# Kernel tuning notes

Hardware: AMD Instinct MI355X
Metric: run time of the kernel (lower is better)

## Reference

```python
import jax, jax.numpy as jnp
import numpy as np


def _lstm(x, h0, c0, Wih, Whh, b):
    """Single-layer LSTM, batch_first input x: [B,T,D]. PyTorch gate order i,f,g,o.
    Returns (h_seq [T,B,H], h_T [B,H], c_T [B,H])."""
    xs = jnp.swapaxes(x, 0, 1)  # [T,B,D]

    def step(carry, xt):
        h, c = carry
        gates = xt @ Wih.T + h @ Whh.T + b  # [B,4H]
        i, f, g, o = jnp.split(gates, 4, axis=-1)
        c = jax.nn.sigmoid(f) * c + jax.nn.sigmoid(i) * jnp.tanh(g)
        h = jax.nn.sigmoid(o) * jnp.tanh(c)
        return (h, c), h

    (h, c), hs = jax.lax.scan(step, (h0, c0), xs)
    return hs, h, c


def setup_inputs() -> dict:
    key = jax.random.key(0)
    ks = jax.random.split(key, 16)
    B, T, Tf, Tu = 256, 365, 15, 76
    Dh, Df, Du, H = 64, 32, 16, 256
    s = 1.0 / np.sqrt(H)  # torch-style uniform scale, approximated with scaled normals
    return {
        "x_d": jax.random.normal(ks[0], (B, T, Dh), jnp.float32),
        "x_f": jax.random.normal(ks[1], (B, Tf, Df), jnp.float32),
        "x_ff": jax.random.normal(ks[2], (B, Tu, Du), jnp.float32),
        "enc_Wih": jax.random.normal(ks[3], (4 * H, Dh), jnp.float32) * s,
        "enc_Whh": jax.random.normal(ks[4], (4 * H, H), jnp.float32) * s,
        "enc_b": jax.random.normal(ks[5], (4 * H,), jnp.float32) * s,
        "decf_Wih": jax.random.normal(ks[6], (4 * H, Df), jnp.float32) * s,
        "decf_Whh": jax.random.normal(ks[7], (4 * H, H), jnp.float32) * s,
        "decf_b": jax.random.normal(ks[8], (4 * H,), jnp.float32) * s,
        "decu_Wih": jax.random.normal(ks[9], (4 * H, Du), jnp.float32) * s,
        "decu_Whh": jax.random.normal(ks[10], (4 * H, H), jnp.float32) * s,
        "decu_b": jax.random.normal(ks[11], (4 * H,), jnp.float32) * s,
        "head_W": jax.random.normal(ks[12], (1, H), jnp.float32) * s,
        "head_b": jax.random.normal(ks[13], (1,), jnp.float32) * s,
    }


def reference(x_d, x_f, x_ff, enc_Wih, enc_Whh, enc_b,
              decf_Wih, decf_Whh, decf_b, decu_Wih, decu_Whh, decu_b,
              head_W, head_b):
    B = x_d.shape[0]
    H = enc_Whh.shape[1]
    Tf = x_f.shape[1]
    Tu = x_ff.shape[1]
    horizon = Tf + Tu
    h0 = jnp.zeros((B, H), x_d.dtype)
    c0 = jnp.zeros((B, H), x_d.dtype)

    # Encoder over historical sequence
    _, h, c = _lstm(x_d, h0, c0, enc_Wih, enc_Whh, enc_b)

    # Forecast decoder: one LSTM step per horizon step + linear head (dropout = eval identity)
    hs_f, h, c = _lstm(x_f, h, c, decf_Wih, decf_Whh, decf_b)  # [Tf,B,H]
    out_f = (jnp.einsum('tbh,oh->tbo', hs_f, head_W)[..., 0] + head_b[0]).T  # [B,Tf]

    # Future decoder, continuing the hidden state
    hs_u, h, c = _lstm(x_ff, h, c, decu_Wih, decu_Whh, decu_b)  # [Tu,B,H]
    out_u = (jnp.einsum('tbh,oh->tbo', hs_u, head_W)[..., 0] + head_b[0]).T  # [B,Tu]

    # Faithful to original: both loops write outputs[:, t], so the future loop
    # overwrites the first Tu columns.
    outputs = jnp.zeros((B, horizon), x_d.dtype)
    outputs = outputs.at[:, :Tf].set(out_f)
    outputs = outputs.at[:, :Tu].set(out_u)
    return outputs
```

## Files before the change

kernel.cpp:

```cpp
#include <hip/hip_runtime.h>
#include <stdint.h>


typedef __attribute__((ext_vector_type(8))) short short8;
typedef __attribute__((ext_vector_type(4))) float f32x4;
typedef __attribute__((ext_vector_type(2))) unsigned int u32x2;

#define L2E 1.4426950408889634f

__device__ __forceinline__ uint16_t f2bf(float f) {
  uint32_t x = __float_as_uint(f);
  x += 0x7fffu + ((x >> 16) & 1u);
  return (uint16_t)(x >> 16);
}
__device__ __forceinline__ uint32_t pk2(float a, float b) {
  return (uint32_t)f2bf(a) | ((uint32_t)f2bf(b) << 16);
}
__device__ __forceinline__ uint32_t cvtpk(float lo, float hi) {
  uint32_t r;
  asm("v_cvt_pk_bf16_f32 %0, %1, %2" : "=v"(r) : "v"(lo), "v"(hi));
  return r;
}
__device__ __forceinline__ float bfhalf(uint32_t w, int hi) {
  return __uint_as_float(hi ? (w & 0xffff0000u) : (w << 16));
}
__device__ __forceinline__ f32x4 MFMA(short8 a, short8 b, f32x4 c) {
  return __builtin_amdgcn_mfma_f32_16x16x32_bf16(a, b, c, 0, 0, 0);
}
__device__ __forceinline__ float ex2(float x) { return __builtin_amdgcn_exp2f(x); }
__device__ __forceinline__ float rcp(float x) { return __builtin_amdgcn_rcpf(x); }

__device__ __forceinline__ void lgkm_barrier() {
  __builtin_amdgcn_sched_barrier(0);
  asm volatile("s_waitcnt lgkmcnt(0)" ::: "memory");
  __builtin_amdgcn_s_barrier();
  __builtin_amdgcn_sched_barrier(0);
}
__device__ __forceinline__ void vm_drain4() {
  __builtin_amdgcn_sched_barrier(0);
  asm volatile("s_waitcnt vmcnt(4)" ::: "memory");
  __builtin_amdgcn_sched_barrier(0);
}

__global__ void init_kernel(float* c_state, uint16_t* h_state, float* out,
                            uint32_t* flags) {
  int i = blockIdx.x * 256 + threadIdx.x;
  if (i < 65536) { c_state[i] = 0.f; h_state[i] = 0; }
  if (i < 256 * 91) out[i] = 0.f;
  if (i < 96) flags[i] = 0;
}

template <int DIN>
__global__ __launch_bounds__(512) void xproj_kernel(
    const float* __restrict__ x, const float* __restrict__ Wih,
    const float* __restrict__ bias, uint32_t* __restrict__ xp,
    int t0, int T) {
  const int tid = threadIdx.x, w = tid >> 6, l = tid & 63;
  const int l16 = l & 15, lg = l >> 4;
  const int tc = blockIdx.x >> 1;
  const int sub = blockIdx.x & 1;
  const int t = t0 + tc;
  constexpr int KT = (DIN + 31) / 32;

  short8 bfr[8][KT];
  float4 bias4[8];
#pragma unroll
  for (int ni = 0; ni < 8; ++ni) {
    const int n = (w * 8 + ni) * 16 + l16;
    bias4[ni] = *(const float4*)&bias[(w * 8 + ni) * 16 + lg * 4];
#pragma unroll
    for (int kt = 0; kt < KT; ++kt) {
      const int k0 = kt * 32 + lg * 8;
      short8 fr;
#pragma unroll
      for (int e = 0; e < 8; ++e) fr[e] = 0;
      if (k0 + 8 <= DIN) {
        const float* s = Wih + (size_t)n * DIN + k0;
#pragma unroll
        for (int e = 0; e < 8; ++e) fr[e] = (short)f2bf(s[e]);
      }
      bfr[ni][kt] = fr;
    }
  }

  for (int mi = 0; mi < 8; ++mi) {
    const int btile = sub * 8 + mi;
    const int b = btile * 16 + l16;
    short8 af[KT];
#pragma unroll
    for (int kt = 0; kt < KT; ++kt) {
      const int k0 = kt * 32 + lg * 8;
      short8 fr;
#pragma unroll
      for (int e = 0; e < 8; ++e) fr[e] = 0;
      if (k0 + 8 <= DIN) {
        const float* s = x + ((size_t)b * T + t) * DIN + k0;
#pragma unroll
        for (int e = 0; e < 8; ++e) fr[e] = (short)f2bf(s[e]);
      }
      af[kt] = fr;
    }
#pragma unroll
    for (int ni = 0; ni < 8; ++ni) {
      f32x4 acc = {0.f, 0.f, 0.f, 0.f};
#pragma unroll
      for (int kt = 0; kt < KT; ++kt) acc = MFMA(bfr[ni][kt], af[kt], acc);
      const int nt = w * 8 + ni;
      const float sc = ((nt >> 4) == 2) ? (2.f * L2E) : -L2E;
      size_t idx = ((((size_t)tc * 16 + btile) * 64 + nt) * 64 + l) * 2;
      u32x2 v;
      v[0] = pk2((acc[0] + bias4[ni].x) * sc, (acc[1] + bias4[ni].y) * sc);
      v[1] = pk2((acc[2] + bias4[ni].z) * sc, (acc[3] + bias4[ni].w) * sc);
      *(u32x2*)(xp + idx) = v;
    }
  }
}

template <int DO_HEAD>
__global__ __launch_bounds__(512, 2) void rec_kernel(
    const uint32_t* __restrict__ xp, const float* __restrict__ Whh,
    float* __restrict__ c_state, uint16_t* __restrict__ h_state,
    float* __restrict__ out, const float* __restrict__ headW,
    const float* __restrict__ headb, uint32_t* __restrict__ flags,
    unsigned long long* __restrict__ hx, uint32_t* __restrict__ hxh,
    int ct, int t0, int phase) {
  __shared__ short8 B_lds[64 * 64];
  __shared__ uint16_t h_lds[2][16][264];
  __shared__ float headbuf[16][8];

  const int tid = threadIdx.x, w = tid >> 6, l = tid & 63;
  const int l16 = l & 15, lg = l >> 4;
  const int blk = blockIdx.x;
  const int pair = blk & 15, s = blk >> 4, sp = 1 - s;
  const int b0 = pair * 16;
  const int ctile = s * 8 + w;
  uint32_t* const pflag = flags + (phase * 16 + pair) * 2 + sp;
  uint32_t* const myflag = flags + (phase * 16 + pair) * 2 + s;

  short8 bv[24];
#pragma unroll
  for (int g = 0; g < 4; ++g) {
    const float wsc = (g == 2) ? (2.f * L2E) : -L2E;
#pragma unroll
    for (int kk = 0; kk < 8; ++kk) {
      const int kt = (kk < 4) ? (4 * s + kk) : (4 * sp + (kk - 4));
      const int row = (g * 16 + ctile) * 16 + l16;
      const float* sw = Whh + (size_t)row * 256 + kt * 32 + lg * 8;
      short8 fr;
#pragma unroll
      for (int e = 0; e < 8; ++e) fr[e] = (short)f2bf(sw[e] * wsc);
      if (kk <= 5) bv[g * 6 + kk] = fr;
      else B_lds[(w * 8 + g * 2 + (kk - 6)) * 64 + l] = fr;
    }
  }

  float c_reg[4];
  {
    float4 c4 = *(const float4*)&c_state[(size_t)(b0 + l16) * 256 +
                                         ctile * 16 + lg * 4];
    c_reg[0] = c4.x; c_reg[1] = c4.y; c_reg[2] = c4.z; c_reg[3] = c4.w;
  }
  for (int idx = tid; idx < 16 * 256; idx += 512)
    h_lds[0][idx >> 8][idx & 255] = h_state[(size_t)(b0 + (idx >> 8)) * 256 + (idx & 255)];
  float4 hw4 = *(const float4*)&headW[ctile * 16 + lg * 4];
  const float hb = headb[0];

  const uint32_t* xpb = xp + ((size_t)(pair * 64 + ctile) * 64 + l) * 2;
  u32x2 xpf[4];
#pragma unroll
  for (int g = 0; g < 4; ++g)
    xpf[g] = *(const u32x2*)(xpb + (size_t)g * 2048);

  __syncthreads();

  u32x2 h_last;
  h_last[0] = 0; h_last[1] = 0;
  float hsum_prev = 0.f;

  for (int t = 0; t < ct; ++t) {
    const int cur = t & 1, nxt = cur ^ 1;
    const int tn = (t + 1 < ct) ? t + 1 : t;
    const int par = t & 1;

    unsigned long long pv = 0ull;
    if (t > 0) {
      const uint32_t tgt = (uint32_t)(t0 + t);
      __builtin_amdgcn_sched_barrier(0);
      uint32_t f;
      do {
        f = __hip_atomic_load(pflag, __ATOMIC_RELAXED, __HIP_MEMORY_SCOPE_AGENT);
      } while ((int)(f - tgt) < 0);
      __builtin_amdgcn_sched_barrier(0);
      pv = __hip_atomic_load(
          hx + ((size_t)((pair * 2 + sp) * 2 + ((t - 1) & 1)) * 512) +
              (w * 4 + lg) * 16 + l16,
          __ATOMIC_RELAXED, __HIP_MEMORY_SCOPE_AGENT);
      if (DO_HEAD && s == 0 && tid < 16) {
        uint32_t pp = __hip_atomic_load(
            hxh + ((pair * 2 + sp) * 2 + ((t - 1) & 1)) * 16 + tid,
            __ATOMIC_RELAXED, __HIP_MEMORY_SCOPE_AGENT);
        out[(size_t)(b0 + tid) * 91 + (t0 + t - 1)] =
            hsum_prev + __uint_as_float(pp) + hb;
      }
    }

    f32x4 acc[4];
#pragma unroll
    for (int g = 0; g < 4; ++g) {
      f32x4 ai;
      ai[0] = bfhalf(xpf[g][0], 0);
      ai[1] = bfhalf(xpf[g][0], 1);
      ai[2] = bfhalf(xpf[g][1], 0);
      ai[3] = bfhalf(xpf[g][1], 1);
      acc[g] = ai;
    }
#pragma unroll
    for (int kk = 0; kk < 4; ++kk) {
      short8 hf = *(const short8*)(&h_lds[cur][l16][(4 * s + kk) * 32 + lg * 8]);
#pragma unroll
      for (int g = 0; g < 4; ++g)
        acc[g] = MFMA(bv[g * 6 + kk], hf, acc[g]);
    }

    if (t > 0) {
      u32x2 pw;
      pw[0] = (uint32_t)pv;
      pw[1] = (uint32_t)(pv >> 32);
      *(u32x2*)(&h_lds[cur][l16][sp * 128 + w * 16 + lg * 4]) = pw;
      lgkm_barrier();
    }

#pragma unroll
    for (int kk = 0; kk < 4; ++kk) {
      short8 hf = *(const short8*)(&h_lds[cur][l16][(4 * sp + kk) * 32 + lg * 8]);
#pragma unroll
      for (int g = 0; g < 4; ++g) {
        if (kk < 2) acc[g] = MFMA(bv[g * 6 + 4 + kk], hf, acc[g]);
        else acc[g] = MFMA(B_lds[(w * 8 + g * 2 + (kk - 2)) * 64 + l], hf, acc[g]);
      }
    }

    float hv[4];
#pragma unroll
    for (int j = 0; j < 4; ++j) {
      float ei = ex2(acc[0][j]);
      float ef = ex2(acc[1][j]);
      float eg = ex2(acc[2][j]);
      float eo = ex2(acc[3][j]);
      float eip = 1.f + ei, egp = eg + 1.f, efp = 1.f + ef;
      float d1 = eip * egp;
      float R = rcp(d1 * efp);
      float sitg = (eg - 1.f) * efp * R;
      float cc = fmaf(c_reg[j] * d1, R, sitg);
      c_reg[j] = cc;
      float ec = ex2(cc * (2.f * L2E));
      float hh = (ec - 1.f) * rcp((1.f + eo) * (ec + 1.f));
      hv[j] = hh;
    }

    h_last[0] = cvtpk(hv[0], hv[1]);
    h_last[1] = cvtpk(hv[2], hv[3]);
    *(u32x2*)(&h_lds[nxt][l16][ctile * 16 + lg * 4]) = h_last;
    {
      unsigned long long v64 =
          ((unsigned long long)h_last[1] << 32) | (unsigned long long)h_last[0];
      __hip_atomic_store(
          hx + ((size_t)((pair * 2 + s) * 2 + par) * 512) + (w * 4 + lg) * 16 + l16,
          v64, __ATOMIC_RELAXED, __HIP_MEMORY_SCOPE_AGENT);
    }

#pragma unroll
    for (int g = 0; g < 4; ++g)
      xpf[g] = *(const u32x2*)(xpb + (size_t)tn * 131072 + g * 2048);

    if (DO_HEAD) {
      float hp = fmaf(hv[0], hw4.x, fmaf(hv[1], hw4.y,
                 fmaf(hv[2], hw4.z, hv[3] * hw4.w)));
      hp += __shfl_xor(hp, 16);
      hp += __shfl_xor(hp, 32);
      if (lg == 0) headbuf[l16][w] = hp;
    }

    vm_drain4();
    lgkm_barrier();

    if (DO_HEAD) {
      if (tid < 16) {
        const float* hbp = headbuf[tid];
        hsum_prev = hbp[0] + hbp[1] + hbp[2] + hbp[3] +
                    hbp[4] + hbp[5] + hbp[6] + hbp[7];
        __hip_atomic_store(hxh + ((pair * 2 + s) * 2 + par) * 16 + tid,
                           __float_as_uint(hsum_prev), __ATOMIC_RELAXED,
                           __HIP_MEMORY_SCOPE_AGENT);
      }
      vm_drain4();
    }
    if (tid == 0)
      __hip_atomic_store(myflag, (uint32_t)(t0 + t + 1), __ATOMIC_RELAXED,
                         __HIP_MEMORY_SCOPE_AGENT);
  }

  {
    float4 c4 = {c_reg[0], c_reg[1], c_reg[2], c_reg[3]};
    *(float4*)&c_state[(size_t)(b0 + l16) * 256 + ctile * 16 + lg * 4] = c4;
  }

  if (s == 0) {
    const uint32_t tgt = (uint32_t)(t0 + ct);
    __builtin_amdgcn_sched_barrier(0);
    uint32_t f;
    do {
      f = __hip_atomic_load(pflag, __ATOMIC_RELAXED, __HIP_MEMORY_SCOPE_AGENT);
    } while ((int)(f - tgt) < 0);
    __builtin_amdgcn_sched_barrier(0);
    unsigned long long pv = __hip_atomic_load(
        hx + ((size_t)((pair * 2 + sp) * 2 + ((ct - 1) & 1)) * 512) +
            (w * 4 + lg) * 16 + l16,
        __ATOMIC_RELAXED, __HIP_MEMORY_SCOPE_AGENT);
    u32x2 pw;
    pw[0] = (uint32_t)pv;
    pw[1] = (uint32_t)(pv >> 32);
    *(u32x2*)&h_state[(size_t)(b0 + l16) * 256 + 128 + w * 16 + lg * 4] = pw;
    *(u32x2*)&h_state[(size_t)(b0 + l16) * 256 + w * 16 + lg * 4] = h_last;
    if (DO_HEAD && tid < 16) {
      uint32_t pp = __hip_atomic_load(
          hxh + ((pair * 2 + sp) * 2 + ((ct - 1) & 1)) * 16 + tid,
          __ATOMIC_RELAXED, __HIP_MEMORY_SCOPE_AGENT);
      out[(size_t)(b0 + tid) * 91 + (t0 + ct - 1)] =
          hsum_prev + __uint_as_float(pp) + hb;
    }
  }
}

extern "C" void kernel_launch(void* const* d_in, const int* in_sizes, int n_in,
                              void* d_out, int out_size, void* d_ws, size_t ws_size,
                              hipStream_t stream) {
  const float* headW = (const float*)d_in[12];
  const float* headb = (const float*)d_in[13];
  float* out = (float*)d_out;

  char* ws = (char*)d_ws;
  float* c_state = (float*)ws;
  uint16_t* h_state = (uint16_t*)(ws + 262144);
  uint32_t* flags = (uint32_t*)(ws + 393216);
  unsigned long long* hx = (unsigned long long*)(ws + 397312);
  uint32_t* hxh = (uint32_t*)(ws + 659456);
  uint32_t* xp = (uint32_t*)(ws + 667648);

  int ct_max = 1;
  if (ws_size > 667648 + 512 * 1024) {
    size_t c = (ws_size - 667648) / (512 * 1024);
    ct_max = (c > 365) ? 365 : (int)c;
  }

  init_kernel<<<256, 256, 0, stream>>>(c_state, h_state, out, flags);

  struct Phase { const float* x; const float* Wih; const float* Whh; const float* b; int T; int D; int head; };
  Phase ph[3] = {
      {(const float*)d_in[0], (const float*)d_in[3], (const float*)d_in[4], (const float*)d_in[5],
       in_sizes[0] / (256 * 64), 64, 0},
      {(const float*)d_in[1], (const float*)d_in[6], (const float*)d_in[7], (const float*)d_in[8],
       in_sizes[1] / (256 * 32), 32, 0},
      {(const float*)d_in[2], (const float*)d_in[9], (const float*)d_in[10], (const float*)d_in[11],
       in_sizes[2] / (256 * 16), 16, 1},
  };

  for (int pi = 0; pi < 3; ++pi) {
    const Phase& P = ph[pi];
    for (int t0 = 0; t0 < P.T; t0 += ct_max) {
      int ct = (P.T - t0 < ct_max) ? (P.T - t0) : ct_max;
      dim3 g(ct * 2);
      if (P.D == 64)
        xproj_kernel<64><<<g, 512, 0, stream>>>(P.x, P.Wih, P.b, xp, t0, P.T);
      else if (P.D == 32)
        xproj_kernel<32><<<g, 512, 0, stream>>>(P.x, P.Wih, P.b, xp, t0, P.T);
      else
        xproj_kernel<16><<<g, 512, 0, stream>>>(P.x, P.Wih, P.b, xp, t0, P.T);
      if (P.head)
        rec_kernel<1><<<32, 512, 0, stream>>>(xp, P.Whh, c_state, h_state, out,
                                              headW, headb, flags, hx, hxh,
                                              ct, t0, pi);
      else
        rec_kernel<0><<<32, 512, 0, stream>>>(xp, P.Whh, c_state, h_state, out,
                                              headW, headb, flags, hx, hxh,
                                              ct, t0, pi);
    }
  }
}
```

Baseline: 1.248 ms.

## Run encoder recurrence on single-block-per-batch-tile kernel without cross-block flags

Adds a new recurrence kernel in which one 512-thread block owns a 16-row batch tile and computes all 1024 gate columns itself. Most of W_hh is held in registers, two K-tiles live in LDS, and h is exchanged only through LDS double buffering. This removes the inter-block flag handshake of the split version for the long encoder phase. When workspace allows, all three input projections are precomputed up front, and the decoders keep the split kernel. The input-projection packing also switches to vectorized float4 loads with the hardware bf16 convert. The trade-off is half the blocks (16 instead of 32), so each block carries twice the MFMA work per step and more register pressure.

```diff
diff --git a/kernel.cpp b/kernel.cpp
--- a/kernel.cpp
+++ b/kernel.cpp
@@ -5,6 +5,7 @@
 typedef __attribute__((ext_vector_type(8))) short short8;
 typedef __attribute__((ext_vector_type(4))) float f32x4;
 typedef __attribute__((ext_vector_type(2))) unsigned int u32x2;
+typedef __attribute__((ext_vector_type(4))) unsigned int u32x4;
 
 #define L2E 1.4426950408889634f
 
@@ -13,9 +14,6 @@
   x += 0x7fffu + ((x >> 16) & 1u);
   return (uint16_t)(x >> 16);
 }
-__device__ __forceinline__ uint32_t pk2(float a, float b) {
-  return (uint32_t)f2bf(a) | ((uint32_t)f2bf(b) << 16);
-}
 __device__ __forceinline__ uint32_t cvtpk(float lo, float hi) {
   uint32_t r;
   asm("v_cvt_pk_bf16_f32 %0, %1, %2" : "=v"(r) : "v"(lo), "v"(hi));
@@ -29,6 +27,16 @@
 }
 __device__ __forceinline__ float ex2(float x) { return __builtin_amdgcn_exp2f(x); }
 __device__ __forceinline__ float rcp(float x) { return __builtin_amdgcn_rcpf(x); }
+
+__device__ __forceinline__ short8 pack8s(const float* s, float sc) {
+  float4 q0 = *(const float4*)s, q1 = *(const float4*)(s + 4);
+  u32x4 t;
+  t[0] = cvtpk(q0.x * sc, q0.y * sc);
+  t[1] = cvtpk(q0.z * sc, q0.w * sc);
+  t[2] = cvtpk(q1.x * sc, q1.y * sc);
+  t[3] = cvtpk(q1.z * sc, q1.w * sc);
+  return *(short8*)&t;
+}
 
 __device__ __forceinline__ void lgkm_barrier() {
   __builtin_amdgcn_sched_barrier(0);
@@ -47,7 +55,7 @@
   int i = blockIdx.x * 256 + threadIdx.x;
   if (i < 65536) { c_state[i] = 0.f; h_state[i] = 0; }
   if (i < 256 * 91) out[i] = 0.f;
-  if (i < 96) flags[i] = 0;
+  if (flags && i < 96) flags[i] = 0;
 }
 
 template <int DIN>
@@ -74,11 +82,7 @@
       short8 fr;
 #pragma unroll
       for (int e = 0; e < 8; ++e) fr[e] = 0;
-      if (k0 + 8 <= DIN) {
-        const float* s = Wih + (size_t)n * DIN + k0;
-#pragma unroll
-        for (int e = 0; e < 8; ++e) fr[e] = (short)f2bf(s[e]);
-      }
+      if (k0 + 8 <= DIN) fr = pack8s(Wih + (size_t)n * DIN + k0, 1.f);
       bfr[ni][kt] = fr;
     }
   }
@@ -93,11 +97,7 @@
       short8 fr;
 #pragma unroll
       for (int e = 0; e < 8; ++e) fr[e] = 0;
-      if (k0 + 8 <= DIN) {
-        const float* s = x + ((size_t)b * T + t) * DIN + k0;
-#pragma unroll
-        for (int e = 0; e < 8; ++e) fr[e] = (short)f2bf(s[e]);
-      }
+      if (k0 + 8 <= DIN) fr = pack8s(x + ((size_t)b * T + t) * DIN + k0, 1.f);
       af[kt] = fr;
     }
 #pragma unroll
@@ -109,8 +109,8 @@
       const float sc = ((nt >> 4) == 2) ? (2.f * L2E) : -L2E;
       size_t idx = ((((size_t)tc * 16 + btile) * 64 + nt) * 64 + l) * 2;
       u32x2 v;
-      v[0] = pk2((acc[0] + bias4[ni].x) * sc, (acc[1] + bias4[ni].y) * sc);
-      v[1] = pk2((acc[2] + bias4[ni].z) * sc, (acc[3] + bias4[ni].w) * sc);
+      v[0] = cvtpk((acc[0] + bias4[ni].x) * sc, (acc[1] + bias4[ni].y) * sc);
+      v[1] = cvtpk((acc[2] + bias4[ni].z) * sc, (acc[3] + bias4[ni].w) * sc);
       *(u32x2*)(xp + idx) = v;
     }
   }
@@ -118,6 +118,156 @@
 
 template <int DO_HEAD>
 __global__ __launch_bounds__(512, 2) void rec_kernel(
+    const uint32_t* __restrict__ xp, const float* __restrict__ Whh,
+    float* __restrict__ c_state, uint16_t* __restrict__ h_state,
+    float* __restrict__ out, const float* __restrict__ headW,
+    const float* __restrict__ headb, int ct, int tcol0) {
+  __shared__ short8 B_lds[8 * 16 * 64];
+  __shared__ uint16_t h_lds[2][16][264];
+  __shared__ float headbuf[2][16][8];
+
+  const int tid = threadIdx.x, w = tid >> 6, l = tid & 63;
+  const int l16 = l & 15, lg = l >> 4;
+  const int blk = blockIdx.x, b0 = blk * 16;
+
+  short8 bv[48];
+#pragma unroll
+  for (int g = 0; g < 4; ++g) {
+    const float wsc = (g == 2) ? (2.f * L2E) : -L2E;
+#pragma unroll
+    for (int nt = 0; nt < 2; ++nt)
+#pragma unroll
+      for (int kt = 0; kt < 8; ++kt) {
+        const int row = (g * 16 + w * 2 + nt) * 16 + l16;
+        const float* s = Whh + (size_t)row * 256 + kt * 32 + lg * 8;
+        short8 fr;
+#pragma unroll
+        for (int e = 0; e < 8; ++e) fr[e] = (short)f2bf(s[e] * wsc);
+        const int tile = g * 2 + nt;
+        if (kt <= 5) bv[tile * 6 + kt] = fr;
+        else B_lds[(w * 16 + (kt - 6) * 8 + tile) * 64 + l] = fr;
+      }
+  }
+
+  float c_reg[2][4];
+#pragma unroll
+  for (int nt = 0; nt < 2; ++nt) {
+    float4 c4 = *(const float4*)&c_state[(size_t)(b0 + l16) * 256 +
+                                         (w * 2 + nt) * 16 + lg * 4];
+    c_reg[nt][0] = c4.x; c_reg[nt][1] = c4.y;
+    c_reg[nt][2] = c4.z; c_reg[nt][3] = c4.w;
+  }
+  for (int idx = tid; idx < 16 * 256; idx += 512)
+    h_lds[0][idx >> 8][idx & 255] = h_state[(size_t)(b0 + (idx >> 8)) * 256 + (idx & 255)];
+  float4 hw4[2];
+#pragma unroll
+  for (int nt = 0; nt < 2; ++nt)
+    hw4[nt] = *(const float4*)&headW[(w * 2 + nt) * 16 + lg * 4];
+  const float hb = headb[0];
+
+  const uint32_t* xpb = xp + ((size_t)(blk * 64 + w * 2) * 64 + l) * 2;
+  u32x2 xpf[2][4];
+#pragma unroll
+  for (int nt = 0; nt < 2; ++nt)
+#pragma unroll
+    for (int g = 0; g < 4; ++g)
+      xpf[nt][g] = *(const u32x2*)(xpb + (size_t)g * 2048 + nt * 128);
+
+  __syncthreads();
+
+  for (int t = 0; t < ct; ++t) {
+    const int cur = t & 1, nxt = cur ^ 1;
+    const int tn = (t + 1 < ct) ? t + 1 : t;
+    float hp = 0.f;
+
+#pragma unroll
+    for (int nt = 0; nt < 2; ++nt) {
+      f32x4 acc[4];
+#pragma unroll
+      for (int g = 0; g < 4; ++g) {
+        f32x4 ai;
+        ai[0] = bfhalf(xpf[nt][g][0], 0);
+        ai[1] = bfhalf(xpf[nt][g][0], 1);
+        ai[2] = bfhalf(xpf[nt][g][1], 0);
+        ai[3] = bfhalf(xpf[nt][g][1], 1);
+        acc[g] = ai;
+      }
+#pragma unroll
+      for (int kt = 0; kt <= 5; ++kt) {
+        short8 hf = *(const short8*)(&h_lds[cur][l16][kt * 32 + lg * 8]);
+#pragma unroll
+        for (int g = 0; g < 4; ++g)
+          acc[g] = MFMA(bv[(g * 2 + nt) * 6 + kt], hf, acc[g]);
+      }
+#pragma unroll
+      for (int kt = 6; kt <= 7; ++kt) {
+        short8 hf = *(const short8*)(&h_lds[cur][l16][kt * 32 + lg * 8]);
+#pragma unroll
+        for (int g = 0; g < 4; ++g)
+          acc[g] = MFMA(B_lds[(w * 16 + (kt - 6) * 8 + g * 2 + nt) * 64 + l], hf, acc[g]);
+      }
+
+      float hv[4];
+#pragma unroll
+      for (int j = 0; j < 4; ++j) {
+        float ei = ex2(acc[0][j]);
+        float ef = ex2(acc[1][j]);
+        float eg = ex2(acc[2][j]);
+        float eo = ex2(acc[3][j]);
+        float eip = 1.f + ei, egp = eg + 1.f, efp = 1.f + ef;
+        float d1 = eip * egp;
+        float R = rcp(d1 * efp);
+        float sitg = (eg - 1.f) * efp * R;
+        float cc = fmaf(c_reg[nt][j] * d1, R, sitg);
+        c_reg[nt][j] = cc;
+        float ec = ex2(cc * (2.f * L2E));
+        float hh = (ec - 1.f) * rcp((1.f + eo) * (ec + 1.f));
+        hv[j] = hh;
+      }
+      if (DO_HEAD) {
+        hp = fmaf(hv[0], hw4[nt].x, hp); hp = fmaf(hv[1], hw4[nt].y, hp);
+        hp = fmaf(hv[2], hw4[nt].z, hp); hp = fmaf(hv[3], hw4[nt].w, hp);
+      }
+      {
+        u32x2 hwrd;
+        hwrd[0] = cvtpk(hv[0], hv[1]);
+        hwrd[1] = cvtpk(hv[2], hv[3]);
+        *(u32x2*)(&h_lds[nxt][l16][(w * 2 + nt) * 16 + lg * 4]) = hwrd;
+      }
+#pragma unroll
+      for (int g = 0; g < 4; ++g)
+        xpf[nt][g] = *(const u32x2*)(xpb + (size_t)tn * 131072 + g * 2048 + nt * 128);
+    }
+
+    if (DO_HEAD) {
+      float s = hp;
+      s += __shfl_xor(s, 16);
+      s += __shfl_xor(s, 32);
+      if (lg == 0) headbuf[t & 1][l16][w] = s;
+    }
+
+    lgkm_barrier();
+
+    if (DO_HEAD) {
+      if (tid < 16) {
+        const float* hbp = headbuf[t & 1][tid];
+        float s = hbp[0] + hbp[1] + hbp[2] + hbp[3] + hbp[4] + hbp[5] + hbp[6] + hbp[7];
+        out[(size_t)(b0 + tid) * 91 + (tcol0 + t)] = s + hb;
+      }
+    }
+  }
+
+#pragma unroll
+  for (int nt = 0; nt < 2; ++nt) {
+    float4 c4 = {c_reg[nt][0], c_reg[nt][1], c_reg[nt][2], c_reg[nt][3]};
+    *(float4*)&c_state[(size_t)(b0 + l16) * 256 + (w * 2 + nt) * 16 + lg * 4] = c4;
+  }
+  for (int idx = tid; idx < 16 * 256; idx += 512)
+    h_state[(size_t)(b0 + (idx >> 8)) * 256 + (idx & 255)] = h_lds[ct & 1][idx >> 8][idx & 255];
+}
+
+template <int DO_HEAD>
+__global__ __launch_bounds__(512, 2) void rec_split(
     const uint32_t* __restrict__ xp, const float* __restrict__ Whh,
     float* __restrict__ c_state, uint16_t* __restrict__ h_state,
     float* __restrict__ out, const float* __restrict__ headW,
@@ -338,31 +488,59 @@
   const float* headW = (const float*)d_in[12];
   const float* headb = (const float*)d_in[13];
   float* out = (float*)d_out;
-
   char* ws = (char*)d_ws;
+
+  const int T0 = in_sizes[0] / (256 * 64);
+  const int T1 = in_sizes[1] / (256 * 32);
+  const int T2 = in_sizes[2] / (256 * 16);
+  const size_t s0 = (size_t)T0 << 19, s1 = (size_t)T1 << 19, s2 = (size_t)T2 << 19;
+  const size_t hdr = 667648;
+
+  if (ws_size >= hdr + s0 + s1 + s2) {
+    float* c_state = (float*)ws;
+    uint16_t* h_state = (uint16_t*)(ws + 262144);
+    uint32_t* flags = (uint32_t*)(ws + 393216);
+    unsigned long long* hx = (unsigned long long*)(ws + 397312);
+    uint32_t* hxh = (uint32_t*)(ws + 659456);
+    uint32_t* xp0 = (uint32_t*)(ws + hdr);
+    uint32_t* xp1 = (uint32_t*)(ws + hdr + s0);
+    uint32_t* xp2 = (uint32_t*)(ws + hdr + s0 + s1);
+
+    init_kernel<<<256, 256, 0, stream>>>(c_state, h_state, out, flags);
+    xproj_kernel<64><<<dim3(T0 * 2), 512, 0, stream>>>(
+        (const float*)d_in[0], (const float*)d_in[3], (const float*)d_in[5], xp0, 0, T0);
+    xproj_kernel<32><<<dim3(T1 * 2), 512, 0, stream>>>(
+        (const float*)d_in[1], (const float*)d_in[6], (const float*)d_in[8], xp1, 0, T1);
+    xproj_kernel<16><<<dim3(T2 * 2), 512, 0, stream>>>(
+        (const float*)d_in[2], (const float*)d_in[9], (const float*)d_in[11], xp2, 0, T2);
+    rec_kernel<0><<<16, 512, 0, stream>>>(xp0, (const float*)d_in[4], c_state,
+                                          h_state, out, headW, headb, T0, 0);
+    rec_split<0><<<32, 512, 0, stream>>>(xp1, (const float*)d_in[7], c_state,
+                                         h_state, out, headW, headb, flags, hx,
+                                         hxh, T1, 0, 1);
+    rec_split<1><<<32, 512, 0, stream>>>(xp2, (const float*)d_in[10], c_state,
+                                         h_state, out, headW, headb, flags, hx,
+                                         hxh, T2, 0, 2);
+    return;
+  }
+
   float* c_state = (float*)ws;
   uint16_t* h_state = (uint16_t*)(ws + 262144);
-  uint32_t* flags = (uint32_t*)(ws + 393216);
-  unsigned long long* hx = (unsigned long long*)(ws + 397312);
-  uint32_t* hxh = (uint32_t*)(ws + 659456);
-  uint32_t* xp = (uint32_t*)(ws + 667648);
+  uint32_t* xp = (uint32_t*)(ws + 393216);
 
   int ct_max = 1;
-  if (ws_size > 667648 + 512 * 1024) {
-    size_t c = (ws_size - 667648) / (512 * 1024);
+  if (ws_size > 393216 + 512 * 1024) {
+    size_t c = (ws_size - 393216) / (512 * 1024);
     ct_max = (c > 365) ? 365 : (int)c;
   }
 
-  init_kernel<<<256, 256, 0, stream>>>(c_state, h_state, out, flags);
+  init_kernel<<<256, 256, 0, stream>>>(c_state, h_state, out, nullptr);
 
   struct Phase { const float* x; const float* Wih; const float* Whh; const float* b; int T; int D; int head; };
   Phase ph[3] = {
-      {(const float*)d_in[0], (const float*)d_in[3], (const float*)d_in[4], (const float*)d_in[5],
-       in_sizes[0] / (256 * 64), 64, 0},
-      {(const float*)d_in[1], (const float*)d_in[6], (const float*)d_in[7], (const float*)d_in[8],
-       in_sizes[1] / (256 * 32), 32, 0},
-      {(const float*)d_in[2], (const float*)d_in[9], (const float*)d_in[10], (const float*)d_in[11],
-       in_sizes[2] / (256 * 16), 16, 1},
+      {(const float*)d_in[0], (const float*)d_in[3], (const float*)d_in[4], (const float*)d_in[5], T0, 64, 0},
+      {(const float*)d_in[1], (const float*)d_in[6], (const float*)d_in[7], (const float*)d_in[8], T1, 32, 0},
+      {(const float*)d_in[2], (const float*)d_in[9], (const float*)d_in[10], (const float*)d_in[11], T2, 16, 1},
   };
 
   for (int pi = 0; pi < 3; ++pi) {
@@ -377,13 +555,11 @@
       else
         xproj_kernel<16><<<g, 512, 0, stream>>>(P.x, P.Wih, P.b, xp, t0, P.T);
       if (P.head)
-        rec_kernel<1><<<32, 512, 0, stream>>>(xp, P.Whh, c_state, h_state, out,
-                                              headW, headb, flags, hx, hxh,
-                                              ct, t0, pi);
+        rec_kernel<1><<<16, 512, 0, stream>>>(xp, P.Whh, c_state, h_state, out,
+                                              headW, headb, ct, t0);
       else
-        rec_kernel<0><<<32, 512, 0, stream>>>(xp, P.Whh, c_state, h_state, out,
-                                              headW, headb, flags, hx, hxh,
-                                              ct, t0, pi);
-    }
-  }
-}
+        rec_kernel<0><<<16, 512, 0, stream>>>(xp, P.Whh, c_state, h_state, out,
+                                              headW, headb, ct, t0);
+    }
+  }
+}
```

Measured after the change: 1.243 ms. Within noise of the previous version (-0.5%).
